# Kernel optimization log

Hardware: AMD Instinct MI355X
Metric: run time of the kernel (lower is better)

Reference implementation:

```python
import jax, jax.numpy as jnp
import numpy as np

B, V, E, L, D = 16, 19, 361, 256, 64  # batch, vertices, edges/graph, seq_len, d_model
F_IN = 2 * D + 1  # concat(src_feat, tgt_feat, edge_weight)


def _linear_init(key, fan_in, fan_out):
    bound = 1.0 / np.sqrt(fan_in)
    kw, kb = jax.random.split(key)
    W = jax.random.uniform(kw, (fan_in, fan_out), jnp.float32, -bound, bound)
    b = jax.random.uniform(kb, (fan_out,), jnp.float32, -bound, bound)
    return W, b


def setup_inputs() -> dict:
    key = jax.random.key(0)
    ks = jax.random.split(key, 6)
    hidden_states = jax.random.normal(ks[0], (B * V, L, D), jnp.float32)
    edge_index = jax.random.randint(ks[1], (2, B * E, L), 0, B * V, dtype=jnp.int32)
    edge_weight = jax.random.uniform(ks[2], (B * E, L), jnp.float32)
    W1, b1 = _linear_init(ks[3], F_IN, D)
    W2, b2 = _linear_init(ks[4], D, D // 2)
    W3, b3 = _linear_init(ks[5], D // 2, 1)
    skip_param = jnp.float32(0.25)
    return {"hidden_states": hidden_states, "edge_weight": edge_weight,
            "W1": W1, "b1": b1, "W2": W2, "b2": b2, "W3": W3, "b3": b3,
            "skip_param": skip_param, "edge_index": edge_index}


def reference(hidden_states, edge_weight, W1, b1, W2, b2, W3, b3, skip_param, edge_index):
    # hidden_states: (B*V, L, D) -> (B, L, V, D) for per-timestep node gather
    hs = hidden_states.reshape(B, V, L, D).transpose(0, 2, 1, 3)
    # edge indices are global node ids; local vertex id = idx % V (as in torch code)
    src = (edge_index[0] % V).reshape(B, E, L).transpose(0, 2, 1)  # (B, L, E)
    tgt = (edge_index[1] % V).reshape(B, E, L).transpose(0, 2, 1)
    ew = edge_weight.reshape(B, E, L).transpose(0, 2, 1)           # (B, L, E)
    src_feat = jnp.take_along_axis(hs, src[..., None], axis=2)    # (B, L, E, D)
    tgt_feat = jnp.take_along_axis(hs, tgt[..., None], axis=2)    # (B, L, E, D)
    x = jnp.concatenate([src_feat, tgt_feat, ew[..., None]], axis=-1)  # (B, L, E, 2D+1)
    h = jax.nn.silu(x @ W1 + b1)
    h = jax.nn.silu(h @ W2 + b2)
    w = jax.nn.sigmoid((h @ W3 + b3)[..., 0])                     # (B, L, E)
    new_ew = skip_param * ew + (1.0 - skip_param) * w
    return new_ew.transpose(0, 2, 1).reshape(B * E, L)            # (B*E, L)
```

## Files before the change

### kernel.cpp

```cpp
#include <hip/hip_runtime.h>

#define NB 16
#define NV 19
#define NE 361
#define NL 256
#define ND 64
#define NT 23
#define NEP (NT * 16)
#define ASTRIDE 136

typedef __attribute__((ext_vector_type(8))) short bf16x8;
typedef __attribute__((ext_vector_type(4))) float f32x4;
typedef __attribute__((ext_vector_type(2))) __bf16 bf16v2;

union bf8u { unsigned u[4]; bf16x8 v; uint4 q; };

__device__ __forceinline__ unsigned pack_bf16(float lo, float hi) {
    bf16v2 v; v.x = (__bf16)lo; v.y = (__bf16)hi;
    return __builtin_bit_cast(unsigned, v);
}
__device__ __forceinline__ short f2bf(float f) {
    __bf16 h = (__bf16)f;
    return __builtin_bit_cast(short, h);
}
__device__ __forceinline__ float bflo(unsigned u) {
    return __builtin_bit_cast(float, u << 16);
}
__device__ __forceinline__ float bfhi(unsigned u) {
    return __builtin_bit_cast(float, u & 0xffff0000u);
}
__device__ __forceinline__ float silu(float x) {
    return x * __builtin_amdgcn_rcpf(1.f + __expf(-x));
}
__device__ __forceinline__ float sigm(float x) {
    return __builtin_amdgcn_rcpf(1.f + __expf(-x));
}

__global__ __launch_bounds__(256, 4) void edge_learner_kernel(
    const float* __restrict__ hs,
    const float* __restrict__ ew_in,
    const float* __restrict__ W1,
    const float* __restrict__ b1,
    const float* __restrict__ W2,
    const float* __restrict__ b2,
    const float* __restrict__ W3,
    const float* __restrict__ b3,
    const float* __restrict__ skip_p,
    const int*   __restrict__ eidx,
    float* __restrict__ out)
{
    __shared__ __align__(16) short A_s[NV * ASTRIDE];
    __shared__ int   srco_s[NEP];
    __shared__ int   tgto_s[NEP];
    __shared__ float ew_s[NEP];

    const int tid  = threadIdx.x;
    const int lane = tid & 63;
    const int wave = tid >> 6;
    const int lq   = lane >> 4;
    const int lm   = lane & 15;
    const int bid  = blockIdx.x;
    const int b    = bid >> 8;
    const int l    = bid & 255;

    for (int e = tid; e < NEP; e += 256) {
        if (e < NE) {
            size_t row = (size_t)(b * NE + e) * NL + l;
            srco_s[e] = (eidx[row] % NV) * ASTRIDE;
            tgto_s[e] = (eidx[(size_t)NB * NE * NL + row] % NV) * ASTRIDE + 64;
            ew_s[e]   = ew_in[row];
        } else {
            srco_s[e] = 0; tgto_s[e] = 64; ew_s[e] = 0.f;
        }
    }

    float w1l_r[16], b1_r[16];
    #pragma unroll
    for (int ks = 0; ks < 2; ++ks)
        #pragma unroll
        for (int i = 0; i < 8; ++i) {
            int ch = ks * 32 + lq * 8 + i;
            w1l_r[ks * 8 + i] = W1[128 * 64 + ch];
            b1_r[ks * 8 + i]  = b1[ch];
        }
    bf16x8 w2f[2][2];
    #pragma unroll
    for (int nt = 0; nt < 2; ++nt)
        #pragma unroll
        for (int ks = 0; ks < 2; ++ks)
            #pragma unroll
            for (int i = 0; i < 8; ++i)
                w2f[nt][ks][i] = f2bf(W2[(ks * 32 + lq * 8 + i) * 32 + nt * 16 + lm]);
    const float b2r0 = b2[lm],      b2r1 = b2[16 + lm];
    const float w3a  = W3[lm],      w3b  = W3[16 + lm];
    const float b3v  = b3[0];
    const float skip = skip_p[0];

    {
        const int half = wave >> 1;
        const int oc0  = (wave & 1) * 32;
        bf16x8 w1f[2][2];
        #pragma unroll
        for (int nt = 0; nt < 2; ++nt)
            #pragma unroll
            for (int ks = 0; ks < 2; ++ks)
                #pragma unroll
                for (int i = 0; i < 8; ++i)
                    w1f[nt][ks][i] = f2bf(
                        W1[(half * 64 + ks * 32 + lq * 8 + i) * 64 + oc0 + nt * 16 + lm]);

        f32x4 acc00 = {0,0,0,0}, acc01 = {0,0,0,0}, acc10 = {0,0,0,0}, acc11 = {0,0,0,0};
        #pragma unroll
        for (int Mt = 0; Mt < 2; ++Mt) {
            int v  = Mt * 16 + lm;
            int vc = v < NV ? v : NV - 1;
            const float* hp = hs + ((size_t)(b * NV + vc) * NL + l) * ND;
            bf8u af[2];
            #pragma unroll
            for (int ks = 0; ks < 2; ++ks) {
                float4 x0 = *(const float4*)&hp[ks * 32 + lq * 8];
                float4 x1 = *(const float4*)&hp[ks * 32 + lq * 8 + 4];
                af[ks].u[0] = pack_bf16(x0.x, x0.y);
                af[ks].u[1] = pack_bf16(x0.z, x0.w);
                af[ks].u[2] = pack_bf16(x1.x, x1.y);
                af[ks].u[3] = pack_bf16(x1.z, x1.w);
            }
            if (Mt == 0) {
                acc00 = __builtin_amdgcn_mfma_f32_16x16x32_bf16(af[0].v, w1f[0][0], acc00, 0, 0, 0);
                acc00 = __builtin_amdgcn_mfma_f32_16x16x32_bf16(af[1].v, w1f[0][1], acc00, 0, 0, 0);
                acc01 = __builtin_amdgcn_mfma_f32_16x16x32_bf16(af[0].v, w1f[1][0], acc01, 0, 0, 0);
                acc01 = __builtin_amdgcn_mfma_f32_16x16x32_bf16(af[1].v, w1f[1][1], acc01, 0, 0, 0);
            } else {
                acc10 = __builtin_amdgcn_mfma_f32_16x16x32_bf16(af[0].v, w1f[0][0], acc10, 0, 0, 0);
                acc10 = __builtin_amdgcn_mfma_f32_16x16x32_bf16(af[1].v, w1f[0][1], acc10, 0, 0, 0);
                acc11 = __builtin_amdgcn_mfma_f32_16x16x32_bf16(af[0].v, w1f[1][0], acc11, 0, 0, 0);
                acc11 = __builtin_amdgcn_mfma_f32_16x16x32_bf16(af[1].v, w1f[1][1], acc11, 0, 0, 0);
            }
        }
        #pragma unroll
        for (int r = 0; r < 4; ++r) {
            int v0 = lq * 4 + r;
            A_s[v0 * ASTRIDE + wave * 32 + lm]      = f2bf(acc00[r]);
            A_s[v0 * ASTRIDE + wave * 32 + 16 + lm] = f2bf(acc01[r]);
            int v1 = 16 + lq * 4 + r;
            if (v1 < NV) {
                A_s[v1 * ASTRIDE + wave * 32 + lm]      = f2bf(acc10[r]);
                A_s[v1 * ASTRIDE + wave * 32 + 16 + lm] = f2bf(acc11[r]);
            }
        }
    }
    __syncthreads();

    for (int t = wave; t < NT; t += 4) {
        const int ebase = t * 16;
        const int e  = ebase + lm;
        const int so = srco_s[e];
        const int to = tgto_s[e];
        const float ew = ew_s[e];

        bf8u a1[2];
        #pragma unroll
        for (int ks = 0; ks < 2; ++ks) {
            bf8u as, at;
            as.q = *(const uint4*)&A_s[so + ks * 32 + lq * 8];
            at.q = *(const uint4*)&A_s[to + ks * 32 + lq * 8];
            #pragma unroll
            for (int p = 0; p < 4; ++p) {
                int ci = ks * 8 + 2 * p;
                float x0 = bflo(as.u[p]) + bflo(at.u[p])
                         + fmaf(ew, w1l_r[ci],     b1_r[ci]);
                float x1 = bfhi(as.u[p]) + bfhi(at.u[p])
                         + fmaf(ew, w1l_r[ci + 1], b1_r[ci + 1]);
                a1[ks].u[p] = pack_bf16(silu(x0), silu(x1));
            }
        }

        f32x4 c0 = {0,0,0,0}, c1 = {0,0,0,0};
        c0 = __builtin_amdgcn_mfma_f32_16x16x32_bf16(a1[0].v, w2f[0][0], c0, 0, 0, 0);
        c0 = __builtin_amdgcn_mfma_f32_16x16x32_bf16(a1[1].v, w2f[0][1], c0, 0, 0, 0);
        c1 = __builtin_amdgcn_mfma_f32_16x16x32_bf16(a1[0].v, w2f[1][0], c1, 0, 0, 0);
        c1 = __builtin_amdgcn_mfma_f32_16x16x32_bf16(a1[1].v, w2f[1][1], c1, 0, 0, 0);

        float p0 = silu(c0[0] + b2r0) * w3a + silu(c1[0] + b2r1) * w3b;
        float p1 = silu(c0[1] + b2r0) * w3a + silu(c1[1] + b2r1) * w3b;
        float p2 = silu(c0[2] + b2r0) * w3a + silu(c1[2] + b2r1) * w3b;
        float p3 = silu(c0[3] + b2r0) * w3a + silu(c1[3] + b2r1) * w3b;

        #pragma unroll
        for (int s = 1; s < 16; s <<= 1) {
            p0 += __shfl_xor(p0, s);
            p1 += __shfl_xor(p1, s);
            p2 += __shfl_xor(p2, s);
            p3 += __shfl_xor(p3, s);
        }
        if (lm < 4) {
            int er = ebase + lq * 4 + (lane & 3);
            if (er < NE) {
                float ps = (lane & 2) ? ((lane & 1) ? p3 : p2)
                                      : ((lane & 1) ? p1 : p0);
                float wgt = sigm(ps + b3v);
                float ewr = ew_s[er];
                out[(size_t)(b * NE + er) * NL + l] = skip * ewr + (1.f - skip) * wgt;
            }
        }
    }
}

extern "C" void kernel_launch(void* const* d_in, const int* in_sizes, int n_in,
                              void* d_out, int out_size, void* d_ws, size_t ws_size,
                              hipStream_t stream) {
    const float* hs   = (const float*)d_in[0];
    const float* ew   = (const float*)d_in[1];
    const float* W1   = (const float*)d_in[2];
    const float* b1   = (const float*)d_in[3];
    const float* W2   = (const float*)d_in[4];
    const float* b2   = (const float*)d_in[5];
    const float* W3   = (const float*)d_in[6];
    const float* b3   = (const float*)d_in[7];
    const float* skip = (const float*)d_in[8];
    const int*   eidx = (const int*)d_in[9];
    float* outp = (float*)d_out;

    dim3 grid(NB * NL);
    dim3 block(256);
    hipLaunchKernelGGL(edge_learner_kernel, grid, block, 0, stream,
                       hs, ew, W1, b1, W2, b2, W3, b3, skip, eidx, outp);
}
```

Before: 69.83 us.

## Store layer-1 node projections as fp32 in LDS, vectorize SiLU, remap block order

Keeps the per-node W1 projections in shared memory as fp32 instead of bf16, so the edge loop loads float4 pairs and skips the bf16 unpacking. SiLU and sigmoid now use exp2/rcp intrinsics on 4-wide vectors, the weight loads are vectorized, and block indices are permuted so that consecutive blocks map to different batch/timestep groups. The costs are twice the LDS footprint and LDS read traffic per edge, plus a small accuracy change from skipping the intermediate bf16 rounding.

```diff
diff --git a/kernel.cpp b/kernel.cpp
--- a/kernel.cpp
+++ b/kernel.cpp
@@ -7,7 +7,7 @@
 #define ND 64
 #define NT 23
 #define NEP (NT * 16)
-#define ASTRIDE 136
+#define ASTR 132
 
 typedef __attribute__((ext_vector_type(8))) short bf16x8;
 typedef __attribute__((ext_vector_type(4))) float f32x4;
@@ -23,17 +23,23 @@
     __bf16 h = (__bf16)f;
     return __builtin_bit_cast(short, h);
 }
-__device__ __forceinline__ float bflo(unsigned u) {
-    return __builtin_bit_cast(float, u << 16);
-}
-__device__ __forceinline__ float bfhi(unsigned u) {
-    return __builtin_bit_cast(float, u & 0xffff0000u);
-}
-__device__ __forceinline__ float silu(float x) {
-    return x * __builtin_amdgcn_rcpf(1.f + __expf(-x));
+__device__ __forceinline__ f32x4 silu4(f32x4 x) {
+    f32x4 t = x * -1.44269504f;
+    f32x4 d;
+    d.x = __builtin_amdgcn_exp2f(t.x);
+    d.y = __builtin_amdgcn_exp2f(t.y);
+    d.z = __builtin_amdgcn_exp2f(t.z);
+    d.w = __builtin_amdgcn_exp2f(t.w);
+    d += 1.f;
+    f32x4 r;
+    r.x = __builtin_amdgcn_rcpf(d.x);
+    r.y = __builtin_amdgcn_rcpf(d.y);
+    r.z = __builtin_amdgcn_rcpf(d.z);
+    r.w = __builtin_amdgcn_rcpf(d.w);
+    return x * r;
 }
 __device__ __forceinline__ float sigm(float x) {
-    return __builtin_amdgcn_rcpf(1.f + __expf(-x));
+    return __builtin_amdgcn_rcpf(1.f + __builtin_amdgcn_exp2f(x * -1.44269504f));
 }
 
 __global__ __launch_bounds__(256, 4) void edge_learner_kernel(
@@ -49,7 +55,7 @@
     const int*   __restrict__ eidx,
     float* __restrict__ out)
 {
-    __shared__ __align__(16) short A_s[NV * ASTRIDE];
+    __shared__ __align__(16) float A_s[NV * ASTR];
     __shared__ int   srco_s[NEP];
     __shared__ int   tgto_s[NEP];
     __shared__ float ew_s[NEP];
@@ -59,38 +65,40 @@
     const int wave = tid >> 6;
     const int lq   = lane >> 4;
     const int lm   = lane & 15;
-    const int bid  = blockIdx.x;
+    const int bid0 = blockIdx.x;
+    const int bid  = (bid0 & 7) * 512 + (bid0 >> 3);
     const int b    = bid >> 8;
     const int l    = bid & 255;
 
     for (int e = tid; e < NEP; e += 256) {
         if (e < NE) {
             size_t row = (size_t)(b * NE + e) * NL + l;
-            srco_s[e] = (eidx[row] % NV) * ASTRIDE;
-            tgto_s[e] = (eidx[(size_t)NB * NE * NL + row] % NV) * ASTRIDE + 64;
+            srco_s[e] = (eidx[row] % NV) * ASTR;
+            tgto_s[e] = (eidx[(size_t)NB * NE * NL + row] % NV) * ASTR + 64;
             ew_s[e]   = ew_in[row];
         } else {
             srco_s[e] = 0; tgto_s[e] = 64; ew_s[e] = 0.f;
         }
     }
 
-    float w1l_r[16], b1_r[16];
+    f32x4 w1lv[2][2], b1v[2][2];
     #pragma unroll
-    for (int ks = 0; ks < 2; ++ks)
-        #pragma unroll
-        for (int i = 0; i < 8; ++i) {
-            int ch = ks * 32 + lq * 8 + i;
-            w1l_r[ks * 8 + i] = W1[128 * 64 + ch];
-            b1_r[ks * 8 + i]  = b1[ch];
-        }
-    bf16x8 w2f[2][2];
+    for (int ks = 0; ks < 2; ++ks) {
+        w1lv[ks][0] = *(const f32x4*)&W1[128 * 64 + ks * 32 + lq * 8];
+        w1lv[ks][1] = *(const f32x4*)&W1[128 * 64 + ks * 32 + lq * 8 + 4];
+        b1v[ks][0]  = *(const f32x4*)&b1[ks * 32 + lq * 8];
+        b1v[ks][1]  = *(const f32x4*)&b1[ks * 32 + lq * 8 + 4];
+    }
+    bf8u w2f[2][2];
     #pragma unroll
     for (int nt = 0; nt < 2; ++nt)
         #pragma unroll
-        for (int ks = 0; ks < 2; ++ks)
+        for (int ks = 0; ks < 2; ++ks) {
+            const float* w2p = &W2[(ks * 32 + lq * 8) * 32 + nt * 16 + lm];
             #pragma unroll
-            for (int i = 0; i < 8; ++i)
-                w2f[nt][ks][i] = f2bf(W2[(ks * 32 + lq * 8 + i) * 32 + nt * 16 + lm]);
+            for (int p = 0; p < 4; ++p)
+                w2f[nt][ks].u[p] = pack_bf16(w2p[(2 * p) * 32], w2p[(2 * p + 1) * 32]);
+        }
     const float b2r0 = b2[lm],      b2r1 = b2[16 + lm];
     const float w3a  = W3[lm],      w3b  = W3[16 + lm];
     const float b3v  = b3[0];
@@ -99,15 +107,17 @@
     {
         const int half = wave >> 1;
         const int oc0  = (wave & 1) * 32;
-        bf16x8 w1f[2][2];
+        bf8u w1f[2][2];
         #pragma unroll
         for (int nt = 0; nt < 2; ++nt)
             #pragma unroll
-            for (int ks = 0; ks < 2; ++ks)
+            for (int ks = 0; ks < 2; ++ks) {
+                const float* wp = &W1[(half * 64 + ks * 32 + lq * 8) * 64
+                                      + oc0 + nt * 16 + lm];
                 #pragma unroll
-                for (int i = 0; i < 8; ++i)
-                    w1f[nt][ks][i] = f2bf(
-                        W1[(half * 64 + ks * 32 + lq * 8 + i) * 64 + oc0 + nt * 16 + lm]);
+                for (int p = 0; p < 4; ++p)
+                    w1f[nt][ks].u[p] = pack_bf16(wp[(2 * p) * 64], wp[(2 * p + 1) * 64]);
+            }
 
         f32x4 acc00 = {0,0,0,0}, acc01 = {0,0,0,0}, acc10 = {0,0,0,0}, acc11 = {0,0,0,0};
         #pragma unroll
@@ -126,26 +136,26 @@
                 af[ks].u[3] = pack_bf16(x1.z, x1.w);
             }
             if (Mt == 0) {
-                acc00 = __builtin_amdgcn_mfma_f32_16x16x32_bf16(af[0].v, w1f[0][0], acc00, 0, 0, 0);
-                acc00 = __builtin_amdgcn_mfma_f32_16x16x32_bf16(af[1].v, w1f[0][1], acc00, 0, 0, 0);
-                acc01 = __builtin_amdgcn_mfma_f32_16x16x32_bf16(af[0].v, w1f[1][0], acc01, 0, 0, 0);
-                acc01 = __builtin_amdgcn_mfma_f32_16x16x32_bf16(af[1].v, w1f[1][1], acc01, 0, 0, 0);
+                acc00 = __builtin_amdgcn_mfma_f32_16x16x32_bf16(af[0].v, w1f[0][0].v, acc00, 0, 0, 0);
+                acc00 = __builtin_amdgcn_mfma_f32_16x16x32_bf16(af[1].v, w1f[0][1].v, acc00, 0, 0, 0);
+                acc01 = __builtin_amdgcn_mfma_f32_16x16x32_bf16(af[0].v, w1f[1][0].v, acc01, 0, 0, 0);
+                acc01 = __builtin_amdgcn_mfma_f32_16x16x32_bf16(af[1].v, w1f[1][1].v, acc01, 0, 0, 0);
             } else {
-                acc10 = __builtin_amdgcn_mfma_f32_16x16x32_bf16(af[0].v, w1f[0][0], acc10, 0, 0, 0);
-                acc10 = __builtin_amdgcn_mfma_f32_16x16x32_bf16(af[1].v, w1f[0][1], acc10, 0, 0, 0);
-                acc11 = __builtin_amdgcn_mfma_f32_16x16x32_bf16(af[0].v, w1f[1][0], acc11, 0, 0, 0);
-                acc11 = __builtin_amdgcn_mfma_f32_16x16x32_bf16(af[1].v, w1f[1][1], acc11, 0, 0, 0);
+                acc10 = __builtin_amdgcn_mfma_f32_16x16x32_bf16(af[0].v, w1f[0][0].v, acc10, 0, 0, 0);
+                acc10 = __builtin_amdgcn_mfma_f32_16x16x32_bf16(af[1].v, w1f[0][1].v, acc10, 0, 0, 0);
+                acc11 = __builtin_amdgcn_mfma_f32_16x16x32_bf16(af[0].v, w1f[1][0].v, acc11, 0, 0, 0);
+                acc11 = __builtin_amdgcn_mfma_f32_16x16x32_bf16(af[1].v, w1f[1][1].v, acc11, 0, 0, 0);
             }
         }
         #pragma unroll
         for (int r = 0; r < 4; ++r) {
             int v0 = lq * 4 + r;
-            A_s[v0 * ASTRIDE + wave * 32 + lm]      = f2bf(acc00[r]);
-            A_s[v0 * ASTRIDE + wave * 32 + 16 + lm] = f2bf(acc01[r]);
+            A_s[v0 * ASTR + wave * 32 + lm]      = acc00[r];
+            A_s[v0 * ASTR + wave * 32 + 16 + lm] = acc01[r];
             int v1 = 16 + lq * 4 + r;
             if (v1 < NV) {
-                A_s[v1 * ASTRIDE + wave * 32 + lm]      = f2bf(acc10[r]);
-                A_s[v1 * ASTRIDE + wave * 32 + 16 + lm] = f2bf(acc11[r]);
+                A_s[v1 * ASTR + wave * 32 + lm]      = acc10[r];
+                A_s[v1 * ASTR + wave * 32 + 16 + lm] = acc11[r];
             }
         }
     }
@@ -158,46 +168,52 @@
         const int to = tgto_s[e];
         const float ew = ew_s[e];
 
+        f32x4 g00 = ew * w1lv[0][0] + b1v[0][0];
+        f32x4 g01 = ew * w1lv[0][1] + b1v[0][1];
+        f32x4 g10 = ew * w1lv[1][0] + b1v[1][0];
+        f32x4 g11 = ew * w1lv[1][1] + b1v[1][1];
+
         bf8u a1[2];
         #pragma unroll
         for (int ks = 0; ks < 2; ++ks) {
-            bf8u as, at;
-            as.q = *(const uint4*)&A_s[so + ks * 32 + lq * 8];
-            at.q = *(const uint4*)&A_s[to + ks * 32 + lq * 8];
-            #pragma unroll
-            for (int p = 0; p < 4; ++p) {
-                int ci = ks * 8 + 2 * p;
-                float x0 = bflo(as.u[p]) + bflo(at.u[p])
-                         + fmaf(ew, w1l_r[ci],     b1_r[ci]);
-                float x1 = bfhi(as.u[p]) + bfhi(at.u[p])
-                         + fmaf(ew, w1l_r[ci + 1], b1_r[ci + 1]);
-                a1[ks].u[p] = pack_bf16(silu(x0), silu(x1));
-            }
+            f32x4 s0 = *(const f32x4*)&A_s[so + ks * 32 + lq * 8];
+            f32x4 s1 = *(const f32x4*)&A_s[so + ks * 32 + lq * 8 + 4];
+            f32x4 t0 = *(const f32x4*)&A_s[to + ks * 32 + lq * 8];
+            f32x4 t1 = *(const f32x4*)&A_s[to + ks * 32 + lq * 8 + 4];
+            f32x4 x0 = s0 + t0 + (ks ? g10 : g00);
+            f32x4 x1 = s1 + t1 + (ks ? g11 : g01);
+            f32x4 y0 = silu4(x0);
+            f32x4 y1 = silu4(x1);
+            a1[ks].u[0] = pack_bf16(y0.x, y0.y);
+            a1[ks].u[1] = pack_bf16(y0.z, y0.w);
+            a1[ks].u[2] = pack_bf16(y1.x, y1.y);
+            a1[ks].u[3] = pack_bf16(y1.z, y1.w);
         }
 
         f32x4 c0 = {0,0,0,0}, c1 = {0,0,0,0};
-        c0 = __builtin_amdgcn_mfma_f32_16x16x32_bf16(a1[0].v, w2f[0][0], c0, 0, 0, 0);
-        c0 = __builtin_amdgcn_mfma_f32_16x16x32_bf16(a1[1].v, w2f[0][1], c0, 0, 0, 0);
-        c1 = __builtin_amdgcn_mfma_f32_16x16x32_bf16(a1[0].v, w2f[1][0], c1, 0, 0, 0);
-        c1 = __builtin_amdgcn_mfma_f32_16x16x32_bf16(a1[1].v, w2f[1][1], c1, 0, 0, 0);
-
-        float p0 = silu(c0[0] + b2r0) * w3a + silu(c1[0] + b2r1) * w3b;
-        float p1 = silu(c0[1] + b2r0) * w3a + silu(c1[1] + b2r1) * w3b;
-        float p2 = silu(c0[2] + b2r0) * w3a + silu(c1[2] + b2r1) * w3b;
-        float p3 = silu(c0[3] + b2r0) * w3a + silu(c1[3] + b2r1) * w3b;
-
+        c0 = __builtin_amdgcn_mfma_f32_16x16x32_bf16(a1[0].v, w2f[0][0].v, c0, 0, 0, 0);
+        c0 = __builtin_amdgcn_mfma_f32_16x16x32_bf16(a1[1].v, w2f[0][1].v, c0, 0, 0, 0);
+        c1 = __builtin_amdgcn_mfma_f32_16x16x32_bf16(a1[0].v, w2f[1][0].v, c1, 0, 0, 0);
+        c1 = __builtin_amdgcn_mfma_f32_16x16x32_bf16(a1[1].v, w2f[1][1].v, c1, 0, 0, 0);
+
+        f32x4 h0 = silu4(c0 + b2r0);
+        f32x4 h1 = silu4(c1 + b2r1);
+        f32x4 p  = h0 * w3a + h1 * w3b;
         #pragma unroll
         for (int s = 1; s < 16; s <<= 1) {
-            p0 += __shfl_xor(p0, s);
-            p1 += __shfl_xor(p1, s);
-            p2 += __shfl_xor(p2, s);
-            p3 += __shfl_xor(p3, s);
+            f32x4 q;
+            q.x = __shfl_xor(p.x, s);
+            q.y = __shfl_xor(p.y, s);
+            q.z = __shfl_xor(p.z, s);
+            q.w = __shfl_xor(p.w, s);
+            p += q;
         }
         if (lm < 4) {
             int er = ebase + lq * 4 + (lane & 3);
             if (er < NE) {
-                float ps = (lane & 2) ? ((lane & 1) ? p3 : p2)
-                                      : ((lane & 1) ? p1 : p0);
+                int r = lane & 3;
+                float ps = (r & 2) ? ((r & 1) ? p.w : p.z)
+                                   : ((r & 1) ? p.y : p.x);
                 float wgt = sigm(ps + b3v);
                 float ewr = ew_s[er];
                 out[(size_t)(b * NE + er) * NL + l] = skip * ewr + (1.f - skip) * wgt;
```

Result: slower. 73.65 us (+5.5%).
